# Kernel optimization log

Hardware: AMD Instinct MI355X
Metric: run time of the kernel (lower is better)

The kernel has to match this reference:

```python
import jax, jax.numpy as jnp
import numpy as np

B, S, H, KVH, D = 1, 2048, 32, 8, 128
ROPE_THETA = 500000.0


def _rotate_half(x):
    x1, x2 = jnp.split(x, 2, axis=-1)
    return jnp.concatenate((-x2, x1), axis=-1)


def setup_inputs() -> dict:
    key = jax.random.key(0)
    ks = jax.random.split(key, 5)
    hidden_states = jax.random.normal(ks[0], (B, S, H * D), dtype=jnp.float32)
    Wq = jax.random.normal(ks[1], (H * D, H * D), dtype=jnp.float32) * 0.02
    Wk = jax.random.normal(ks[2], (KVH * D, H * D), dtype=jnp.float32) * 0.02
    Wv = jax.random.normal(ks[3], (KVH * D, H * D), dtype=jnp.float32) * 0.02
    Wo = jax.random.normal(ks[4], (H * D, H * D), dtype=jnp.float32) * 0.02
    # rotary tables (Llama-style, concat of freqs with itself)
    inv_freq = 1.0 / (ROPE_THETA ** (jnp.arange(0, D, 2, dtype=jnp.float32) / D))
    freqs = jnp.arange(S, dtype=jnp.float32)[:, None] * inv_freq[None, :]  # [S, D/2]
    emb = jnp.concatenate((freqs, freqs), axis=-1)  # [S, D]
    cos = jnp.cos(emb)[None]  # [1, S, D]
    sin = jnp.sin(emb)[None]
    # additive causal mask, matching SDPA attn_mask semantics
    causal = jnp.tril(jnp.ones((S, S), dtype=bool))
    attention_mask = jnp.where(causal, 0.0, -1e9).astype(jnp.float32)[None, None]  # [1,1,S,S]
    return {"hidden_states": hidden_states, "attention_mask": attention_mask,
            "cos": cos, "sin": sin, "Wq": Wq, "Wk": Wk, "Wv": Wv, "Wo": Wo}


def reference(hidden_states, attention_mask, cos, sin, Wq, Wk, Wv, Wo):
    b, s, _ = hidden_states.shape
    d = cos.shape[-1]
    h = Wq.shape[0] // d
    kvh = Wk.shape[0] // d
    g = h // kvh  # GQA group size

    # fused QKV projection (nn.Linear: y = x @ W^T), then split heads -> [b, heads, s, d]
    q = jnp.einsum('bsi,oi->bso', hidden_states, Wq).reshape(b, s, h, d).transpose(0, 2, 1, 3)
    k = jnp.einsum('bsi,oi->bso', hidden_states, Wk).reshape(b, s, kvh, d).transpose(0, 2, 1, 3)
    v = jnp.einsum('bsi,oi->bso', hidden_states, Wv).reshape(b, s, kvh, d).transpose(0, 2, 1, 3)

    # rotary embedding (unsqueeze_dim=1)
    c = cos[:, None]  # [b,1,s,d]
    sn = sin[:, None]
    q = q * c + _rotate_half(q) * sn
    k = k * c + _rotate_half(k) * sn

    # GQA: view q as [b, kvh, g, s, d]; contract against un-repeated k/v
    qg = q.reshape(b, kvh, g, s, d)
    scale = 1.0 / jnp.sqrt(jnp.float32(d))
    scores = jnp.einsum('bkgsd,bktd->bkgst', qg, k) * scale  # [b,kvh,g,s,s]
    scores = scores + attention_mask[:, :, None]  # broadcast [b,1,1,s,s]
    probs = jax.nn.softmax(scores, axis=-1)
    attn = jnp.einsum('bkgst,bktd->bkgsd', probs, v)  # [b,kvh,g,s,d]

    attn = attn.reshape(b, h, s, d).transpose(0, 2, 1, 3).reshape(b, s, h * d)
    out = jnp.einsum('bso,po->bsp', attn, Wo)
    return out
```

## Files before the change

kernel.cpp:

```cpp
#include <hip/hip_runtime.h>
#include <hip/hip_bf16.h>

#define SEQ 2048
#define HD  128
#define NH  32
#define NKV 8
#define MODEL 4096
#define KVDIM 1024
#define QKVN 6144

typedef __attribute__((ext_vector_type(8))) short short8;
typedef __attribute__((ext_vector_type(4))) short short4v;
typedef __attribute__((ext_vector_type(4))) float float4v;

#define MFMA16(a, b, c) __builtin_amdgcn_mfma_f32_16x16x32_bf16(a, b, c, 0, 0, 0)

__device__ __forceinline__ short f2bf(float x) {
  unsigned u = __builtin_bit_cast(unsigned, x);
  u += 0x7fffu + ((u >> 16) & 1u);
  return (short)(u >> 16);
}
__device__ __forceinline__ float bf2f(short s) {
  unsigned u = ((unsigned)(unsigned short)s) << 16;
  return __builtin_bit_cast(float, u);
}

__device__ __forceinline__ void async_copy16(const void* g, void* l) {
  __builtin_amdgcn_global_load_lds((const __attribute__((address_space(1))) void*)g,
                                   (__attribute__((address_space(3))) void*)l, 16, 0, 0);
}

__global__ __launch_bounds__(256) void cast_fused(const float* __restrict__ wq,
                                                  const float* __restrict__ wk,
                                                  const float* __restrict__ wv,
                                                  const float* __restrict__ wo,
                                                  const float* __restrict__ hid,
                                                  short* __restrict__ dst) {
  int b = blockIdx.x;
  const float* src;
  int rbase, lblk;
  if (b < 16384)      { src = wq;  rbase = 0;     lblk = b; }
  else if (b < 20480) { src = wk;  rbase = 16384; lblk = b - 16384; }
  else if (b < 24576) { src = wv;  rbase = 20480; lblk = b - 20480; }
  else if (b < 40960) { src = wo;  rbase = 24576; lblk = b - 24576; }
  else                { src = hid; rbase = 40960; lblk = b - 40960; }
  size_t li = (size_t)lblk * 1024 + threadIdx.x * 4;
  float4v v = *(const float4v*)(src + li);
  short4v o;
  o[0] = f2bf(v[0]); o[1] = f2bf(v[1]); o[2] = f2bf(v[2]); o[3] = f2bf(v[3]);
  *(short4v*)(dst + (size_t)rbase * 1024 + li) = o;
}

__device__ __forceinline__ void store_out(float* C, size_t idx, float v) { C[idx] = v; }
__device__ __forceinline__ void store_out(short* C, size_t idx, float v) { C[idx] = f2bf(v); }

template <int NI, typename OUT>
__global__ __launch_bounds__(512, 2) void gemm256t(const short* __restrict__ A,
                                                   const short* __restrict__ B,
                                                   OUT* __restrict__ C,
                                                   int M, int N, int K) {
  constexpr int BN = NI * 64;
  __shared__ __align__(16) short As[2][256 * 64];
  __shared__ __align__(16) short Bs[2][BN * 64];
  const int tid = threadIdx.x;
  const int lane = tid & 63, w = tid >> 6;
  const int col = lane & 15, quad = lane >> 4;
  const int wm = w >> 2, wn = w & 3;

  const int nbx = N / BN;
  int bid = blockIdx.x, nwg = gridDim.x;
  int swz = (nwg & 7) ? bid : ((bid & 7) * (nwg >> 3) + (bid >> 3));
  const int m0 = (swz / nbx) << 8;
  const int n0 = (swz % nbx) * BN;

  const int srow = tid >> 3;
  const int schunk = (tid & 7) ^ (srow & 7);
  const short* pA = A + (size_t)(m0 + srow) * K + schunk * 8;
  const short* pB = B + (size_t)(n0 + srow) * K + schunk * 8;
  const int ldst = tid * 8;

  const int sw = (col & 7) << 3;
  const int kof0 = (quad * 8) ^ sw;
  const int kof1 = (32 + quad * 8) ^ sw;
  const int ra = wm * 128, rb = wn * (NI * 16);

  float4v acc[8][NI] = {};
  const int iters = K >> 6;

#define SA(buf, rA, kt) async_copy16(pA + (size_t)(rA) * K + (kt), &As[buf][(rA) * 64 + ldst])
#define SB_(buf, rB, kt) async_copy16(pB + (size_t)(rB) * K + (kt), &Bs[buf][(rB) * 64 + ldst])

  SA(0, 0, 0);  SA(0, 128, 0);
  SB_(0, 0, 0); SB_(0, 64, 0);
  if constexpr (NI == 3) SB_(0, 128, 0);
  SA(0, 64, 0); SA(0, 192, 0);
  asm volatile("s_waitcnt vmcnt(2)" ::: "memory");
  __builtin_amdgcn_s_barrier();

  for (int t = 0; t < iters; ++t) {
    const int cb = t & 1, nb = cb ^ 1;
    const int kt = (t + 1) << 6;
    const bool pf = (t + 1 < iters);
    const short* a_ = As[cb];
    const short* b_ = Bs[cb];
    short8 bf[NI][2];
    short8 af[4][2];

#pragma unroll
    for (int j = 0; j < 4; ++j) {
      const short* rp = a_ + (ra + j * 16 + col) * 64;
      af[j][0] = *(const short8*)(rp + kof0);
      af[j][1] = *(const short8*)(rp + kof1);
    }
#pragma unroll
    for (int ni = 0; ni < NI; ++ni) {
      const short* rp = b_ + (rb + ni * 16 + col) * 64;
      bf[ni][0] = *(const short8*)(rp + kof0);
      bf[ni][1] = *(const short8*)(rp + kof1);
    }
    if (pf) { SA(nb, 0, kt); SA(nb, 128, kt); SB_(nb, 0, kt); SB_(nb, 64, kt); }
    __builtin_amdgcn_s_barrier();
    asm volatile("s_waitcnt lgkmcnt(0)" ::: "memory");
    __builtin_amdgcn_sched_barrier(0);
    __builtin_amdgcn_s_setprio(1);
#pragma unroll
    for (int j = 0; j < 4; ++j)
#pragma unroll
      for (int ni = 0; ni < NI; ++ni) {
        acc[j][ni] = MFMA16(af[j][0], bf[ni][0], acc[j][ni]);
        acc[j][ni] = MFMA16(af[j][1], bf[ni][1], acc[j][ni]);
      }
    __builtin_amdgcn_s_setprio(0);
    if (pf) asm volatile("s_waitcnt vmcnt(4)" ::: "memory");
    else    asm volatile("s_waitcnt vmcnt(0)" ::: "memory");
    __builtin_amdgcn_s_barrier();

#pragma unroll
    for (int j = 0; j < 4; ++j) {
      const short* rp = a_ + (ra + (4 + j) * 16 + col) * 64;
      af[j][0] = *(const short8*)(rp + kof0);
      af[j][1] = *(const short8*)(rp + kof1);
    }
    if (pf) {
      if constexpr (NI == 3) SB_(nb, 128, kt);
      SA(nb, 64, kt); SA(nb, 192, kt);
    }
    __builtin_amdgcn_s_barrier();
    asm volatile("s_waitcnt lgkmcnt(0)" ::: "memory");
    __builtin_amdgcn_sched_barrier(0);
    __builtin_amdgcn_s_setprio(1);
#pragma unroll
    for (int j = 0; j < 4; ++j)
#pragma unroll
      for (int ni = 0; ni < NI; ++ni) {
        acc[4 + j][ni] = MFMA16(af[j][0], bf[ni][0], acc[4 + j][ni]);
        acc[4 + j][ni] = MFMA16(af[j][1], bf[ni][1], acc[4 + j][ni]);
      }
    __builtin_amdgcn_s_setprio(0);
    if (pf) asm volatile("s_waitcnt vmcnt(2)" ::: "memory");
    __builtin_amdgcn_s_barrier();
  }
#undef SA
#undef SB_

#pragma unroll
  for (int mi = 0; mi < 8; ++mi)
#pragma unroll
    for (int ni = 0; ni < NI; ++ni)
#pragma unroll
      for (int r = 0; r < 4; ++r) {
        int row = m0 + ra + mi * 16 + quad * 4 + r;
        int cc  = n0 + rb + ni * 16 + col;
        store_out(C, (size_t)row * N + cc, acc[mi][ni][r]);
      }
}

#define BM 128
#define BN 128
#define BK 32

template <typename OUT>
__global__ __launch_bounds__(256) void gemm_nt(const short* __restrict__ A,
                                               const short* __restrict__ B,
                                               OUT* __restrict__ C,
                                               int M, int N, int K) {
  __shared__ __align__(16) short As[2][BM * BK];
  __shared__ __align__(16) short Bs[2][BN * BK];
  int t = threadIdx.x;
  int w = t >> 6, lane = t & 63;
  int col = lane & 15, quad = lane >> 4;
  int m0 = blockIdx.y * BM, n0 = blockIdx.x * BN;
  int wr = (w >> 1) * 64, wc = (w & 1) * 64;

  int srow   = lane >> 2;
  int schunk = (lane & 3) ^ ((lane >> 3) & 3);
  const short* Ag0 = A + (size_t)(m0 + w * 32 + srow) * K + schunk * 8;
  const short* Ag1 = Ag0 + (size_t)16 * K;
  const short* Bg0 = B + (size_t)(n0 + w * 32 + srow) * K + schunk * 8;
  const short* Bg1 = Bg0 + (size_t)16 * K;
  const int wofs0 = (w * 32) * BK;
  const int wofs1 = (w * 32 + 16) * BK;

  int aswz = (quad ^ ((col >> 1) & 3)) * 8;

  float4v acc[4][4] = {};

  async_copy16(Ag0, &As[0][wofs0]);
  async_copy16(Ag1, &As[0][wofs1]);
  async_copy16(Bg0, &Bs[0][wofs0]);
  async_copy16(Bg1, &Bs[0][wofs1]);
  __syncthreads();

  const int iters = K / BK;
  for (int it = 0; it < iters; it++) {
    const int cb = it & 1, nb = cb ^ 1;
    if (it + 1 < iters) {
      const int k0 = (it + 1) * BK;
      async_copy16(Ag0 + k0, &As[nb][wofs0]);
      async_copy16(Ag1 + k0, &As[nb][wofs1]);
      async_copy16(Bg0 + k0, &Bs[nb][wofs0]);
      async_copy16(Bg1 + k0, &Bs[nb][wofs1]);
    }
    short8 af[4], bfr[4];
#pragma unroll
    for (int i = 0; i < 4; i++)
      af[i] = *(const short8*)&As[cb][(wr + i * 16 + col) * BK + aswz];
#pragma unroll
    for (int i = 0; i < 4; i++)
      bfr[i] = *(const short8*)&Bs[cb][(wc + i * 16 + col) * BK + aswz];
#pragma unroll
    for (int mi = 0; mi < 4; mi++)
#pragma unroll
      for (int ni = 0; ni < 4; ni++)
        acc[mi][ni] = MFMA16(af[mi], bfr[ni], acc[mi][ni]);
    __syncthreads();
  }

#pragma unroll
  for (int mi = 0; mi < 4; mi++)
#pragma unroll
    for (int ni = 0; ni < 4; ni++)
#pragma unroll
      for (int r = 0; r < 4; r++) {
        int row = m0 + wr + mi * 16 + quad * 4 + r;
        int cc  = n0 + wc + ni * 16 + col;
        store_out(C, (size_t)row * N + cc, acc[mi][ni][r]);
      }
}

__global__ __launch_bounds__(256) void rope_fused(const short* __restrict__ qkv,
                                                  const float* __restrict__ cosp,
                                                  const float* __restrict__ sinp,
                                                  short* __restrict__ qb,
                                                  short* __restrict__ kb,
                                                  short* __restrict__ vt) {
  __shared__ short tile[32][137];
  const int b = blockIdx.x, t = threadIdx.x;

  if (b < 2560) {
    const bool isq = b < 2048;
    const int bb = isq ? b : b - 2048;
    const int head = bb >> 6;
    const int s = ((bb & 63) << 5) + (t >> 3);
    const int d0 = (t & 7) * 8;
    const int cbase = s * HD + d0;
    float4v c0 = *(const float4v*)(cosp + cbase);
    float4v c1 = *(const float4v*)(cosp + cbase + 4);
    float4v s0v = *(const float4v*)(sinp + cbase);
    float4v s1v = *(const float4v*)(sinp + cbase + 4);
    const short* base = qkv + (size_t)s * QKVN + (isq ? head * HD : MODEL + head * HD) + d0;
    short8 lo = *(const short8*)(base);
    short8 hi = *(const short8*)(base + 64);
    const float scale = isq ? 0.08838834764831845f : 1.0f;
    short8 olo, ohi;
#pragma unroll
    for (int j = 0; j < 8; j++) {
      float c = (j < 4) ? c0[j] : c1[j - 4];
      float sn = (j < 4) ? s0v[j] : s1v[j - 4];
      float l = bf2f(lo[j]), h = bf2f(hi[j]);
      olo[j] = f2bf((l * c - h * sn) * scale);
      ohi[j] = f2bf((h * c + l * sn) * scale);
    }
    short* out = (isq ? qb : kb) + ((size_t)(head * SEQ + s)) * HD + d0;
    *(short8*)(out) = olo;
    *(short8*)(out + 64) = ohi;
  } else {
    const int bb = b - 2560;
    const int kv = bb >> 6;
    const int s0 = (bb & 63) << 5;
    const int lrow = t >> 4, chunk = t & 15;
    const short* src = qkv + (size_t)(s0 + lrow) * QKVN + MODEL + KVDIM + kv * HD + chunk * 8;
#pragma unroll
    for (int rr = 0; rr < 2; rr++)
      *(short8*)&tile[lrow + rr * 16][chunk * 8] =
          *(const short8*)(src + (size_t)rr * 16 * QKVN);
    __syncthreads();
    const int sc = t & 3, d = t >> 2;
#pragma unroll
    for (int dd = 0; dd < 2; dd++) {
      short8 o;
#pragma unroll
      for (int j = 0; j < 8; j++) o[j] = tile[sc * 8 + j][d + dd * 64];
      *(short8*)(vt + ((size_t)(kv * HD + d + dd * 64)) * SEQ + s0 + sc * 8) = o;
    }
  }
}

#define FKT 32
#define KLD 136
#define VLD 40
#define PLD 40

__global__ __launch_bounds__(256, 3) void flash_attn(const short* __restrict__ qb_,
                                                     const short* __restrict__ kb,
                                                     const short* __restrict__ vt,
                                                     short* __restrict__ attn) {
  __shared__ __align__(16) short Ks[2][FKT * KLD];
  __shared__ __align__(16) short Vs[2][HD * VLD];
  __shared__ __align__(16) short Ps[4][32 * PLD];
  const int tid = threadIdx.x;
  const int w = tid >> 6, lane = tid & 63;
  const int col = lane & 15, quad = lane >> 4;
  const int h = blockIdx.x;
  const int kv = h >> 2;
  const int yp = (blockIdx.y < 8) ? (15 - (int)blockIdx.y) : ((int)blockIdx.y - 8);
  const int qB0 = yp * 128;
  const int q0w = qB0 + w * 32;
  const int ntiles = qB0 / FKT + 4;

  short8 ones;
#pragma unroll
  for (int i = 0; i < 8; i++) ones[i] = (short)0x3F80;

  short8 qf[2][4];
  const short* qbase = qb_ + ((size_t)(h * SEQ + q0w + col)) * HD;
#pragma unroll
  for (int rt = 0; rt < 2; rt++)
#pragma unroll
    for (int ks = 0; ks < 4; ks++)
      qf[rt][ks] = *(const short8*)(qbase + rt * 16 * HD + ks * 32 + quad * 8);

  float4v o[2][8] = {};
  float4v la[2] = {};

  const int kg_off = tid * 8;
  const int klds0  = (kg_off >> 7) * KLD + (kg_off & 127);
  const int vd     = tid >> 2;
  const int vkof   = (tid & 3) * 8;
  const size_t vrow0 = ((size_t)(kv * HD + vd)) * SEQ;
  const size_t vrow1 = ((size_t)(kv * HD + vd + 64)) * SEQ;
  const int vlds0 = vd * VLD + vkof;
  const short* kgbase = kb + ((size_t)kv * SEQ) * HD;

  short8 kr0, kr1, vr0, vr1;
  kr0 = *(const short8*)(kgbase + kg_off);
  kr1 = *(const short8*)(kgbase + 2048 + kg_off);
  vr0 = *(const short8*)(vt + vrow0 + vkof);
  vr1 = *(const short8*)(vt + vrow1 + vkof);
  *(short8*)&Ks[0][klds0]            = kr0;
  *(short8*)&Ks[0][klds0 + 16 * KLD] = kr1;
  *(short8*)&Vs[0][vlds0]            = vr0;
  *(short8*)&Vs[0][vlds0 + 64 * VLD] = vr1;
  __syncthreads();

  for (int kt = 0; kt < ntiles; kt++) {
    const int b = kt & 1;
    const int key0 = kt * FKT;
    if (kt + 1 < ntiles) {
      const int nk0 = key0 + FKT;
      const short* kg = kgbase + (size_t)nk0 * HD;
      kr0 = *(const short8*)(kg + kg_off);
      kr1 = *(const short8*)(kg + 2048 + kg_off);
      vr0 = *(const short8*)(vt + vrow0 + nk0 + vkof);
      vr1 = *(const short8*)(vt + vrow1 + nk0 + vkof);
    }
    if (key0 <= q0w + 31) {
      float4v sct[2][2] = {};
#pragma unroll
      for (int ks = 0; ks < 4; ks++) {
        short8 kf0 = *(const short8*)&Ks[b][col * KLD + ks * 32 + quad * 8];
        short8 kf1 = *(const short8*)&Ks[b][(16 + col) * KLD + ks * 32 + quad * 8];
        sct[0][0] = MFMA16(kf0, qf[0][ks], sct[0][0]);
        sct[0][1] = MFMA16(kf0, qf[1][ks], sct[0][1]);
        sct[1][0] = MFMA16(kf1, qf[0][ks], sct[1][0]);
        sct[1][1] = MFMA16(kf1, qf[1][ks], sct[1][1]);
      }
      short* pw = Ps[w];
      if (key0 + 31 <= q0w) {
#pragma unroll
        for (int rt = 0; rt < 2; rt++)
#pragma unroll
          for (int kt2 = 0; kt2 < 2; kt2++) {
            short4v p;
#pragma unroll
            for (int r = 0; r < 4; r++) p[r] = f2bf(__expf(sct[kt2][rt][r]));
            *(short4v*)&pw[(rt * 16 + col) * PLD + kt2 * 16 + quad * 4] = p;
          }
      } else {
#pragma unroll
        for (int rt = 0; rt < 2; rt++) {
          int qrow = q0w + rt * 16 + col;
#pragma unroll
          for (int kt2 = 0; kt2 < 2; kt2++) {
            int keyb = key0 + kt2 * 16 + quad * 4;
            short4v p;
#pragma unroll
            for (int r = 0; r < 4; r++) {
              float s = sct[kt2][rt][r];
              if (keyb + r > qrow) s = -INFINITY;
              p[r] = f2bf(__expf(s));
            }
            *(short4v*)&pw[(rt * 16 + col) * PLD + kt2 * 16 + quad * 4] = p;
          }
        }
      }
      asm volatile("s_waitcnt lgkmcnt(0)" ::: "memory");
      short8 pf0 = *(const short8*)&pw[col * PLD + quad * 8];
      short8 pf1 = *(const short8*)&pw[(16 + col) * PLD + quad * 8];
      la[0] = MFMA16(ones, pf0, la[0]);
      la[1] = MFMA16(ones, pf1, la[1]);
#pragma unroll
      for (int nc = 0; nc < 8; nc++) {
        short8 vb = *(const short8*)&Vs[b][(nc * 16 + col) * VLD + quad * 8];
        o[0][nc] = MFMA16(vb, pf0, o[0][nc]);
        o[1][nc] = MFMA16(vb, pf1, o[1][nc]);
      }
    }
    if (kt + 1 < ntiles) {
      const int nb = 1 - b;
      *(short8*)&Ks[nb][klds0]            = kr0;
      *(short8*)&Ks[nb][klds0 + 16 * KLD] = kr1;
      *(short8*)&Vs[nb][vlds0]            = vr0;
      *(short8*)&Vs[nb][vlds0 + 64 * VLD] = vr1;
    }
    __syncthreads();
  }

#pragma unroll
  for (int rt = 0; rt < 2; rt++) {
    float inv = 1.0f / la[rt][0];
    size_t rowbase = (size_t)(q0w + rt * 16 + col) * MODEL + h * HD + quad * 4;
#pragma unroll
    for (int nc = 0; nc < 8; nc++) {
      short4v ov;
#pragma unroll
      for (int r = 0; r < 4; r++) ov[r] = f2bf(o[rt][nc][r] * inv);
      *(short4v*)(attn + rowbase + nc * 16) = ov;
    }
  }
}

extern "C" void kernel_launch(void* const* d_in, const int* in_sizes, int n_in,
                              void* d_out, int out_size, void* d_ws, size_t ws_size,
                              hipStream_t stream) {
  const float* hidden = (const float*)d_in[0];
  const float* cosp = (const float*)d_in[2];
  const float* sinp = (const float*)d_in[3];
  const float* Wq   = (const float*)d_in[4];
  const float* Wk   = (const float*)d_in[5];
  const float* Wv   = (const float*)d_in[6];
  const float* Wo   = (const float*)d_in[7];

  char* ws = (char*)d_ws;
  size_t off = 0;
  auto alloc = [&](size_t bytes) {
    char* p = ws + off;
    off += (bytes + 255) & ~(size_t)255;
    return p;
  };
  short* wq_bf = (short*)alloc((size_t)MODEL * MODEL * 2);
  short* wk_bf = (short*)alloc((size_t)KVDIM * MODEL * 2);
  short* wv_bf = (short*)alloc((size_t)KVDIM * MODEL * 2);
  short* wo_bf = (short*)alloc((size_t)MODEL * MODEL * 2);
  short* h_bf  = (short*)alloc((size_t)SEQ * MODEL * 2);
  short* qkv_bf = (short*)alloc((size_t)SEQ * QKVN * 2);
  short* k_bf  = (short*)alloc((size_t)NKV * SEQ * HD * 2);
  short* v_t   = (short*)alloc((size_t)NKV * HD * SEQ * 2);
  short* attn_bf = (short*)alloc((size_t)SEQ * MODEL * 2);
  short* q_bf    = h_bf;

  cast_fused<<<49152, 256, 0, stream>>>(Wq, Wk, Wv, Wo, hidden, wq_bf);

  gemm256t<3, short><<<dim3((SEQ / 256) * (QKVN / 192)), 512, 0, stream>>>(
      h_bf, wq_bf, qkv_bf, SEQ, QKVN, MODEL);

  rope_fused<<<3072, 256, 0, stream>>>(qkv_bf, cosp, sinp, q_bf, k_bf, v_t);

  flash_attn<<<dim3(NH, SEQ / 128), 256, 0, stream>>>(q_bf, k_bf, v_t, attn_bf);

  gemm_nt<float><<<dim3(MODEL / BN, SEQ / BM), 256, 0, stream>>>(
      attn_bf, wo_bf, (float*)d_out, SEQ, MODEL, MODEL);
}
```

Measured before the change: 500.3 us.

## Fuse Q rotary into attention Q load and use gemm256t for output projection

Rotary embedding and scaling for Q are now applied inside the attention kernel when Q fragments are loaded directly from the QKV buffer. The separate pass no longer writes a rotated Q buffer, so the rope kernel shrinks to K rotation plus the V transpose. The output projection also switches from the 128x128 gemm_nt kernel to the larger-tile gemm256t template. Together these aim to cut Q write/read traffic and improve output GEMM efficiency. The cost is strided QKV and cos/sin loads in the attention prologue, and a possible change in wave count for the output GEMM.

```diff
diff --git a/kernel.cpp b/kernel.cpp
--- a/kernel.cpp
+++ b/kernel.cpp
@@ -175,117 +175,40 @@
       }
 }
 
-#define BM 128
-#define BN 128
-#define BK 32
-
-template <typename OUT>
-__global__ __launch_bounds__(256) void gemm_nt(const short* __restrict__ A,
-                                               const short* __restrict__ B,
-                                               OUT* __restrict__ C,
-                                               int M, int N, int K) {
-  __shared__ __align__(16) short As[2][BM * BK];
-  __shared__ __align__(16) short Bs[2][BN * BK];
-  int t = threadIdx.x;
-  int w = t >> 6, lane = t & 63;
-  int col = lane & 15, quad = lane >> 4;
-  int m0 = blockIdx.y * BM, n0 = blockIdx.x * BN;
-  int wr = (w >> 1) * 64, wc = (w & 1) * 64;
-
-  int srow   = lane >> 2;
-  int schunk = (lane & 3) ^ ((lane >> 3) & 3);
-  const short* Ag0 = A + (size_t)(m0 + w * 32 + srow) * K + schunk * 8;
-  const short* Ag1 = Ag0 + (size_t)16 * K;
-  const short* Bg0 = B + (size_t)(n0 + w * 32 + srow) * K + schunk * 8;
-  const short* Bg1 = Bg0 + (size_t)16 * K;
-  const int wofs0 = (w * 32) * BK;
-  const int wofs1 = (w * 32 + 16) * BK;
-
-  int aswz = (quad ^ ((col >> 1) & 3)) * 8;
-
-  float4v acc[4][4] = {};
-
-  async_copy16(Ag0, &As[0][wofs0]);
-  async_copy16(Ag1, &As[0][wofs1]);
-  async_copy16(Bg0, &Bs[0][wofs0]);
-  async_copy16(Bg1, &Bs[0][wofs1]);
-  __syncthreads();
-
-  const int iters = K / BK;
-  for (int it = 0; it < iters; it++) {
-    const int cb = it & 1, nb = cb ^ 1;
-    if (it + 1 < iters) {
-      const int k0 = (it + 1) * BK;
-      async_copy16(Ag0 + k0, &As[nb][wofs0]);
-      async_copy16(Ag1 + k0, &As[nb][wofs1]);
-      async_copy16(Bg0 + k0, &Bs[nb][wofs0]);
-      async_copy16(Bg1 + k0, &Bs[nb][wofs1]);
-    }
-    short8 af[4], bfr[4];
-#pragma unroll
-    for (int i = 0; i < 4; i++)
-      af[i] = *(const short8*)&As[cb][(wr + i * 16 + col) * BK + aswz];
-#pragma unroll
-    for (int i = 0; i < 4; i++)
-      bfr[i] = *(const short8*)&Bs[cb][(wc + i * 16 + col) * BK + aswz];
-#pragma unroll
-    for (int mi = 0; mi < 4; mi++)
-#pragma unroll
-      for (int ni = 0; ni < 4; ni++)
-        acc[mi][ni] = MFMA16(af[mi], bfr[ni], acc[mi][ni]);
-    __syncthreads();
-  }
-
-#pragma unroll
-  for (int mi = 0; mi < 4; mi++)
-#pragma unroll
-    for (int ni = 0; ni < 4; ni++)
-#pragma unroll
-      for (int r = 0; r < 4; r++) {
-        int row = m0 + wr + mi * 16 + quad * 4 + r;
-        int cc  = n0 + wc + ni * 16 + col;
-        store_out(C, (size_t)row * N + cc, acc[mi][ni][r]);
-      }
-}
-
-__global__ __launch_bounds__(256) void rope_fused(const short* __restrict__ qkv,
-                                                  const float* __restrict__ cosp,
-                                                  const float* __restrict__ sinp,
-                                                  short* __restrict__ qb,
-                                                  short* __restrict__ kb,
-                                                  short* __restrict__ vt) {
+__global__ __launch_bounds__(256) void ropek_vtrans(const short* __restrict__ qkv,
+                                                    const float* __restrict__ cosp,
+                                                    const float* __restrict__ sinp,
+                                                    short* __restrict__ kb,
+                                                    short* __restrict__ vt) {
   __shared__ short tile[32][137];
   const int b = blockIdx.x, t = threadIdx.x;
 
-  if (b < 2560) {
-    const bool isq = b < 2048;
-    const int bb = isq ? b : b - 2048;
-    const int head = bb >> 6;
-    const int s = ((bb & 63) << 5) + (t >> 3);
+  if (b < 512) {
+    const int head = b >> 6;
+    const int s = ((b & 63) << 5) + (t >> 3);
     const int d0 = (t & 7) * 8;
     const int cbase = s * HD + d0;
     float4v c0 = *(const float4v*)(cosp + cbase);
     float4v c1 = *(const float4v*)(cosp + cbase + 4);
     float4v s0v = *(const float4v*)(sinp + cbase);
     float4v s1v = *(const float4v*)(sinp + cbase + 4);
-    const short* base = qkv + (size_t)s * QKVN + (isq ? head * HD : MODEL + head * HD) + d0;
+    const short* base = qkv + (size_t)s * QKVN + MODEL + head * HD + d0;
     short8 lo = *(const short8*)(base);
     short8 hi = *(const short8*)(base + 64);
-    const float scale = isq ? 0.08838834764831845f : 1.0f;
     short8 olo, ohi;
 #pragma unroll
     for (int j = 0; j < 8; j++) {
       float c = (j < 4) ? c0[j] : c1[j - 4];
       float sn = (j < 4) ? s0v[j] : s1v[j - 4];
       float l = bf2f(lo[j]), h = bf2f(hi[j]);
-      olo[j] = f2bf((l * c - h * sn) * scale);
-      ohi[j] = f2bf((h * c + l * sn) * scale);
-    }
-    short* out = (isq ? qb : kb) + ((size_t)(head * SEQ + s)) * HD + d0;
+      olo[j] = f2bf(l * c - h * sn);
+      ohi[j] = f2bf(h * c + l * sn);
+    }
+    short* out = kb + ((size_t)(head * SEQ + s)) * HD + d0;
     *(short8*)(out) = olo;
     *(short8*)(out + 64) = ohi;
   } else {
-    const int bb = b - 2560;
+    const int bb = b - 512;
     const int kv = bb >> 6;
     const int s0 = (bb & 63) << 5;
     const int lrow = t >> 4, chunk = t & 15;
@@ -311,7 +234,9 @@
 #define VLD 40
 #define PLD 40
 
-__global__ __launch_bounds__(256, 3) void flash_attn(const short* __restrict__ qb_,
+__global__ __launch_bounds__(256, 3) void flash_attn(const short* __restrict__ qkv,
+                                                     const float* __restrict__ cosp,
+                                                     const float* __restrict__ sinp,
                                                      const short* __restrict__ kb,
                                                      const short* __restrict__ vt,
                                                      short* __restrict__ attn) {
@@ -333,12 +258,34 @@
   for (int i = 0; i < 8; i++) ones[i] = (short)0x3F80;
 
   short8 qf[2][4];
-  const short* qbase = qb_ + ((size_t)(h * SEQ + q0w + col)) * HD;
-#pragma unroll
-  for (int rt = 0; rt < 2; rt++)
-#pragma unroll
-    for (int ks = 0; ks < 4; ks++)
-      qf[rt][ks] = *(const short8*)(qbase + rt * 16 * HD + ks * 32 + quad * 8);
+  {
+    const short* qrow0 = qkv + (size_t)(q0w + col) * QKVN + h * HD;
+    const float* cb0 = cosp + (size_t)(q0w + col) * HD;
+    const float* sb0 = sinp + (size_t)(q0w + col) * HD;
+#pragma unroll
+    for (int rt = 0; rt < 2; rt++) {
+      const short* qr = qrow0 + (size_t)rt * 16 * QKVN;
+      const float* cr = cb0 + rt * 16 * HD;
+      const float* sr = sb0 + rt * 16 * HD;
+#pragma unroll
+      for (int ks = 0; ks < 2; ks++) {
+        short8 lo = *(const short8*)(qr + ks * 32 + quad * 8);
+        short8 hi = *(const short8*)(qr + 64 + ks * 32 + quad * 8);
+        const float* cc = cr + ks * 32 + quad * 8;
+        const float* ss = sr + ks * 32 + quad * 8;
+        short8 olo, ohi;
+#pragma unroll
+        for (int j = 0; j < 8; j++) {
+          float c = cc[j], sn = ss[j];
+          float l = bf2f(lo[j]), hh = bf2f(hi[j]);
+          olo[j] = f2bf((l * c - hh * sn) * 0.08838834764831845f);
+          ohi[j] = f2bf((hh * c + l * sn) * 0.08838834764831845f);
+        }
+        qf[rt][ks]     = olo;
+        qf[rt][ks + 2] = ohi;
+      }
+    }
+  }
 
   float4v o[2][8] = {};
   float4v la[2] = {};
@@ -477,17 +424,16 @@
   short* k_bf  = (short*)alloc((size_t)NKV * SEQ * HD * 2);
   short* v_t   = (short*)alloc((size_t)NKV * HD * SEQ * 2);
   short* attn_bf = (short*)alloc((size_t)SEQ * MODEL * 2);
-  short* q_bf    = h_bf;
 
   cast_fused<<<49152, 256, 0, stream>>>(Wq, Wk, Wv, Wo, hidden, wq_bf);
 
   gemm256t<3, short><<<dim3((SEQ / 256) * (QKVN / 192)), 512, 0, stream>>>(
       h_bf, wq_bf, qkv_bf, SEQ, QKVN, MODEL);
 
-  rope_fused<<<3072, 256, 0, stream>>>(qkv_bf, cosp, sinp, q_bf, k_bf, v_t);
-
-  flash_attn<<<dim3(NH, SEQ / 128), 256, 0, stream>>>(q_bf, k_bf, v_t, attn_bf);
-
-  gemm_nt<float><<<dim3(MODEL / BN, SEQ / BM), 256, 0, stream>>>(
+  ropek_vtrans<<<1024, 256, 0, stream>>>(qkv_bf, cosp, sinp, k_bf, v_t);
+
+  flash_attn<<<dim3(NH, SEQ / 128), 256, 0, stream>>>(qkv_bf, cosp, sinp, k_bf, v_t, attn_bf);
+
+  gemm256t<2, float><<<dim3((SEQ / 256) * (MODEL / 128)), 512, 0, stream>>>(
       attn_bf, wo_bf, (float*)d_out, SEQ, MODEL, MODEL);
 }
```

After: 472.9 us (median of 2 runs). -5.5%, faster.

## Fuse Q rotary into flash attention and use 8 waves of 16 query rows

Applied to the files above, without the earlier changes.

Removes the separate Q RoPE pass by loading Q straight from the QKV buffer and applying rotary and scale inside the attention kernel, so the rope kernel now handles only K and the V transpose. The attention block grows to 512 threads with eight waves, each owning 16 query rows instead of 32. This removes one write and read of Q through global memory and gives more waves to hide latency, but halves the register reuse of each K and V shared-memory fragment per wave. Each thread also now loads one K and one V chunk per tile instead of two.

```diff
diff --git a/kernel.cpp b/kernel.cpp
--- a/kernel.cpp
+++ b/kernel.cpp
@@ -248,44 +248,40 @@
       }
 }
 
-__global__ __launch_bounds__(256) void rope_fused(const short* __restrict__ qkv,
-                                                  const float* __restrict__ cosp,
-                                                  const float* __restrict__ sinp,
-                                                  short* __restrict__ qb,
-                                                  short* __restrict__ kb,
-                                                  short* __restrict__ vt) {
+__global__ __launch_bounds__(256) void ropek_vtrans(const short* __restrict__ qkv,
+                                                    const float* __restrict__ cosp,
+                                                    const float* __restrict__ sinp,
+                                                    short* __restrict__ kb,
+                                                    short* __restrict__ vt) {
   __shared__ short tile[32][137];
   const int b = blockIdx.x, t = threadIdx.x;
 
-  if (b < 2560) {
-    const bool isq = b < 2048;
-    const int bb = isq ? b : b - 2048;
-    const int head = bb >> 6;
-    const int s = ((bb & 63) << 5) + (t >> 3);
+  if (b < 512) {
+    const int head = b >> 6;
+    const int s = ((b & 63) << 5) + (t >> 3);
     const int d0 = (t & 7) * 8;
     const int cbase = s * HD + d0;
     float4v c0 = *(const float4v*)(cosp + cbase);
     float4v c1 = *(const float4v*)(cosp + cbase + 4);
     float4v s0v = *(const float4v*)(sinp + cbase);
     float4v s1v = *(const float4v*)(sinp + cbase + 4);
-    const short* base = qkv + (size_t)s * QKVN + (isq ? head * HD : MODEL + head * HD) + d0;
+    const short* base = qkv + (size_t)s * QKVN + MODEL + head * HD + d0;
     short8 lo = *(const short8*)(base);
     short8 hi = *(const short8*)(base + 64);
-    const float scale = isq ? 0.08838834764831845f : 1.0f;
     short8 olo, ohi;
 #pragma unroll
     for (int j = 0; j < 8; j++) {
       float c = (j < 4) ? c0[j] : c1[j - 4];
       float sn = (j < 4) ? s0v[j] : s1v[j - 4];
       float l = bf2f(lo[j]), h = bf2f(hi[j]);
-      olo[j] = f2bf((l * c - h * sn) * scale);
-      ohi[j] = f2bf((h * c + l * sn) * scale);
-    }
-    short* out = (isq ? qb : kb) + ((size_t)(head * SEQ + s)) * HD + d0;
+      olo[j] = f2bf(l * c - h * sn);
+      ohi[j] = f2bf(h * c + l * sn);
+    }
+    short* out = kb + ((size_t)(head * SEQ + s)) * HD + d0;
     *(short8*)(out) = olo;
     *(short8*)(out + 64) = ohi;
   } else {
-    const int bb = b - 2560;
+    const int bb = b - 512;
     const int kv = bb >> 6;
     const int s0 = (bb & 63) << 5;
     const int lrow = t >> 4, chunk = t & 15;
@@ -311,13 +307,15 @@
 #define VLD 40
 #define PLD 40
 
-__global__ __launch_bounds__(256, 3) void flash_attn(const short* __restrict__ qb_,
+__global__ __launch_bounds__(512, 4) void flash_attn(const short* __restrict__ qkv,
+                                                     const float* __restrict__ cosp,
+                                                     const float* __restrict__ sinp,
                                                      const short* __restrict__ kb,
                                                      const short* __restrict__ vt,
                                                      short* __restrict__ attn) {
   __shared__ __align__(16) short Ks[2][FKT * KLD];
   __shared__ __align__(16) short Vs[2][HD * VLD];
-  __shared__ __align__(16) short Ps[4][32 * PLD];
+  __shared__ __align__(16) short Ps[8][16 * PLD];
   const int tid = threadIdx.x;
   const int w = tid >> 6, lane = tid & 63;
   const int col = lane & 15, quad = lane >> 4;
@@ -325,42 +323,54 @@
   const int kv = h >> 2;
   const int yp = (blockIdx.y < 8) ? (15 - (int)blockIdx.y) : ((int)blockIdx.y - 8);
   const int qB0 = yp * 128;
-  const int q0w = qB0 + w * 32;
+  const int q0w = qB0 + w * 16;
   const int ntiles = qB0 / FKT + 4;
 
   short8 ones;
 #pragma unroll
   for (int i = 0; i < 8; i++) ones[i] = (short)0x3F80;
 
-  short8 qf[2][4];
-  const short* qbase = qb_ + ((size_t)(h * SEQ + q0w + col)) * HD;
-#pragma unroll
-  for (int rt = 0; rt < 2; rt++)
-#pragma unroll
-    for (int ks = 0; ks < 4; ks++)
-      qf[rt][ks] = *(const short8*)(qbase + rt * 16 * HD + ks * 32 + quad * 8);
-
-  float4v o[2][8] = {};
-  float4v la[2] = {};
+  short8 qf[4];
+  {
+    const int qrow_g = q0w + col;
+    const short* qr = qkv + (size_t)qrow_g * QKVN + h * HD;
+    const float* cr = cosp + (size_t)qrow_g * HD;
+    const float* sr = sinp + (size_t)qrow_g * HD;
+#pragma unroll
+    for (int ks = 0; ks < 2; ks++) {
+      short8 lo = *(const short8*)(qr + ks * 32 + quad * 8);
+      short8 hi = *(const short8*)(qr + 64 + ks * 32 + quad * 8);
+      const float* cc = cr + ks * 32 + quad * 8;
+      const float* ss = sr + ks * 32 + quad * 8;
+      short8 olo, ohi;
+#pragma unroll
+      for (int j = 0; j < 8; j++) {
+        float c = cc[j], sn = ss[j];
+        float l = bf2f(lo[j]), hh = bf2f(hi[j]);
+        olo[j] = f2bf((l * c - hh * sn) * 0.08838834764831845f);
+        ohi[j] = f2bf((hh * c + l * sn) * 0.08838834764831845f);
+      }
+      qf[ks]     = olo;
+      qf[ks + 2] = ohi;
+    }
+  }
+
+  float4v o[8] = {};
+  float4v la = {};
 
   const int kg_off = tid * 8;
   const int klds0  = (kg_off >> 7) * KLD + (kg_off & 127);
   const int vd     = tid >> 2;
   const int vkof   = (tid & 3) * 8;
-  const size_t vrow0 = ((size_t)(kv * HD + vd)) * SEQ;
-  const size_t vrow1 = ((size_t)(kv * HD + vd + 64)) * SEQ;
-  const int vlds0 = vd * VLD + vkof;
+  const size_t vrow = ((size_t)(kv * HD + vd)) * SEQ;
+  const int vlds = vd * VLD + vkof;
   const short* kgbase = kb + ((size_t)kv * SEQ) * HD;
 
-  short8 kr0, kr1, vr0, vr1;
-  kr0 = *(const short8*)(kgbase + kg_off);
-  kr1 = *(const short8*)(kgbase + 2048 + kg_off);
-  vr0 = *(const short8*)(vt + vrow0 + vkof);
-  vr1 = *(const short8*)(vt + vrow1 + vkof);
-  *(short8*)&Ks[0][klds0]            = kr0;
-  *(short8*)&Ks[0][klds0 + 16 * KLD] = kr1;
-  *(short8*)&Vs[0][vlds0]            = vr0;
-  *(short8*)&Vs[0][vlds0 + 64 * VLD] = vr1;
+  short8 kr, vr;
+  kr = *(const short8*)(kgbase + kg_off);
+  vr = *(const short8*)(vt + vrow + vkof);
+  *(short8*)&Ks[0][klds0] = kr;
+  *(short8*)&Vs[0][vlds]  = vr;
   __syncthreads();
 
   for (int kt = 0; kt < ntiles; kt++) {
@@ -368,83 +378,67 @@
     const int key0 = kt * FKT;
     if (kt + 1 < ntiles) {
       const int nk0 = key0 + FKT;
-      const short* kg = kgbase + (size_t)nk0 * HD;
-      kr0 = *(const short8*)(kg + kg_off);
-      kr1 = *(const short8*)(kg + 2048 + kg_off);
-      vr0 = *(const short8*)(vt + vrow0 + nk0 + vkof);
-      vr1 = *(const short8*)(vt + vrow1 + nk0 + vkof);
-    }
-    if (key0 <= q0w + 31) {
-      float4v sct[2][2] = {};
+      kr = *(const short8*)(kgbase + (size_t)nk0 * HD + kg_off);
+      vr = *(const short8*)(vt + vrow + nk0 + vkof);
+    }
+    if (key0 <= q0w + 15) {
+      float4v sct[2] = {};
 #pragma unroll
       for (int ks = 0; ks < 4; ks++) {
         short8 kf0 = *(const short8*)&Ks[b][col * KLD + ks * 32 + quad * 8];
         short8 kf1 = *(const short8*)&Ks[b][(16 + col) * KLD + ks * 32 + quad * 8];
-        sct[0][0] = MFMA16(kf0, qf[0][ks], sct[0][0]);
-        sct[0][1] = MFMA16(kf0, qf[1][ks], sct[0][1]);
-        sct[1][0] = MFMA16(kf1, qf[0][ks], sct[1][0]);
-        sct[1][1] = MFMA16(kf1, qf[1][ks], sct[1][1]);
+        sct[0] = MFMA16(kf0, qf[ks], sct[0]);
+        sct[1] = MFMA16(kf1, qf[ks], sct[1]);
       }
       short* pw = Ps[w];
       if (key0 + 31 <= q0w) {
 #pragma unroll
-        for (int rt = 0; rt < 2; rt++)
-#pragma unroll
-          for (int kt2 = 0; kt2 < 2; kt2++) {
-            short4v p;
-#pragma unroll
-            for (int r = 0; r < 4; r++) p[r] = f2bf(__expf(sct[kt2][rt][r]));
-            *(short4v*)&pw[(rt * 16 + col) * PLD + kt2 * 16 + quad * 4] = p;
+        for (int kt2 = 0; kt2 < 2; kt2++) {
+          short4v p;
+#pragma unroll
+          for (int r = 0; r < 4; r++) p[r] = f2bf(__expf(sct[kt2][r]));
+          *(short4v*)&pw[col * PLD + kt2 * 16 + quad * 4] = p;
+        }
+      } else {
+        int qrow = q0w + col;
+#pragma unroll
+        for (int kt2 = 0; kt2 < 2; kt2++) {
+          int keyb = key0 + kt2 * 16 + quad * 4;
+          short4v p;
+#pragma unroll
+          for (int r = 0; r < 4; r++) {
+            float s = sct[kt2][r];
+            if (keyb + r > qrow) s = -INFINITY;
+            p[r] = f2bf(__expf(s));
           }
-      } else {
-#pragma unroll
-        for (int rt = 0; rt < 2; rt++) {
-          int qrow = q0w + rt * 16 + col;
-#pragma unroll
-          for (int kt2 = 0; kt2 < 2; kt2++) {
-            int keyb = key0 + kt2 * 16 + quad * 4;
-            short4v p;
-#pragma unroll
-            for (int r = 0; r < 4; r++) {
-              float s = sct[kt2][rt][r];
-              if (keyb + r > qrow) s = -INFINITY;
-              p[r] = f2bf(__expf(s));
-            }
-            *(short4v*)&pw[(rt * 16 + col) * PLD + kt2 * 16 + quad * 4] = p;
-          }
+          *(short4v*)&pw[col * PLD + kt2 * 16 + quad * 4] = p;
         }
       }
       asm volatile("s_waitcnt lgkmcnt(0)" ::: "memory");
-      short8 pf0 = *(const short8*)&pw[col * PLD + quad * 8];
-      short8 pf1 = *(const short8*)&pw[(16 + col) * PLD + quad * 8];
-      la[0] = MFMA16(ones, pf0, la[0]);
-      la[1] = MFMA16(ones, pf1, la[1]);
+      short8 pf = *(const short8*)&pw[col * PLD + quad * 8];
+      la = MFMA16(ones, pf, la);
 #pragma unroll
       for (int nc = 0; nc < 8; nc++) {
         short8 vb = *(const short8*)&Vs[b][(nc * 16 + col) * VLD + quad * 8];
-        o[0][nc] = MFMA16(vb, pf0, o[0][nc]);
-        o[1][nc] = MFMA16(vb, pf1, o[1][nc]);
+        o[nc] = MFMA16(vb, pf, o[nc]);
       }
     }
     if (kt + 1 < ntiles) {
       const int nb = 1 - b;
-      *(short8*)&Ks[nb][klds0]            = kr0;
-      *(short8*)&Ks[nb][klds0 + 16 * KLD] = kr1;
-      *(short8*)&Vs[nb][vlds0]            = vr0;
-      *(short8*)&Vs[nb][vlds0 + 64 * VLD] = vr1;
+      *(short8*)&Ks[nb][klds0] = kr;
+      *(short8*)&Vs[nb][vlds]  = vr;
     }
     __syncthreads();
   }
 
-#pragma unroll
-  for (int rt = 0; rt < 2; rt++) {
-    float inv = 1.0f / la[rt][0];
-    size_t rowbase = (size_t)(q0w + rt * 16 + col) * MODEL + h * HD + quad * 4;
+  {
+    float inv = 1.0f / la[0];
+    size_t rowbase = (size_t)(q0w + col) * MODEL + h * HD + quad * 4;
 #pragma unroll
     for (int nc = 0; nc < 8; nc++) {
       short4v ov;
 #pragma unroll
-      for (int r = 0; r < 4; r++) ov[r] = f2bf(o[rt][nc][r] * inv);
+      for (int r = 0; r < 4; r++) ov[r] = f2bf(o[nc][r] * inv);
       *(short4v*)(attn + rowbase + nc * 16) = ov;
     }
   }
@@ -477,16 +471,15 @@
   short* k_bf  = (short*)alloc((size_t)NKV * SEQ * HD * 2);
   short* v_t   = (short*)alloc((size_t)NKV * HD * SEQ * 2);
   short* attn_bf = (short*)alloc((size_t)SEQ * MODEL * 2);
-  short* q_bf    = h_bf;
 
   cast_fused<<<49152, 256, 0, stream>>>(Wq, Wk, Wv, Wo, hidden, wq_bf);
 
   gemm256t<3, short><<<dim3((SEQ / 256) * (QKVN / 192)), 512, 0, stream>>>(
       h_bf, wq_bf, qkv_bf, SEQ, QKVN, MODEL);
 
-  rope_fused<<<3072, 256, 0, stream>>>(qkv_bf, cosp, sinp, q_bf, k_bf, v_t);
-
-  flash_attn<<<dim3(NH, SEQ / 128), 256, 0, stream>>>(q_bf, k_bf, v_t, attn_bf);
+  ropek_vtrans<<<1024, 256, 0, stream>>>(qkv_bf, cosp, sinp, k_bf, v_t);
+
+  flash_attn<<<dim3(NH, SEQ / 128), 512, 0, stream>>>(qkv_bf, cosp, sinp, k_bf, v_t, attn_bf);
 
   gemm_nt<float><<<dim3(MODEL / BN, SEQ / BM), 256, 0, stream>>>(
       attn_bf, wo_bf, (float*)d_out, SEQ, MODEL, MODEL);
```

Result: faster. 489.1 us (-2.2%).
